# Kernel tuning notes

Measured on AMD Instinct MI355X. Metric: run time of the kernel, lower is better.

Reference implementation:

```python
import jax, jax.numpy as jnp
import numpy as np

N_NODES = 50000
N_EDGES = 800000
IN, HID, OUT = 128, 32, 64
HEADS = (4, 4, 4, 4)  # heads per layer (heads[0], heads[1], heads[1], heads[2])
NEG_SLOPE = 0.2


def gat_layer(h, src, dst, W, al, ar, b, activation):
    """One DGL-style GATConv. h: [N, Din]; W: [Din, H*F]; al, ar: [H, F]; b: [H*F]."""
    n = h.shape[0]
    H, F = al.shape
    feat = (h @ W).reshape(n, H, F)                       # [N, H, F]
    el = jnp.sum(feat * al, axis=-1)                      # [N, H]
    er = jnp.sum(feat * ar, axis=-1)                      # [N, H]
    e = jax.nn.leaky_relu(el[src] + er[dst], NEG_SLOPE)   # [E, H]
    # segment softmax over incoming edges of each dst node
    m = jax.ops.segment_max(e, dst, num_segments=n)       # [N, H]
    ex = jnp.exp(e - m[dst])                              # [E, H]
    denom = jax.ops.segment_sum(ex, dst, num_segments=n)  # [N, H]
    alpha = ex / jnp.maximum(denom[dst], 1e-9)            # [E, H]
    msg = feat[src] * alpha[:, :, None]                   # [E, H, F]
    out = jax.ops.segment_sum(msg, dst, num_segments=n) + b.reshape(H, F)
    return activation(out) if activation is not None else out


def setup_inputs() -> dict:
    key = jax.random.key(0)
    ks = jax.random.split(key, 20)
    x = jax.random.normal(ks[0], (N_NODES, IN), dtype=jnp.float32)
    src = jax.random.randint(ks[1], (N_EDGES,), 0, N_NODES, dtype=jnp.int32)
    dst = jax.random.randint(ks[2], (N_EDGES,), 0, N_NODES, dtype=jnp.int32)
    dims = [(IN, HEADS[0], HID), (HID * HEADS[0], HEADS[1], HID),
            (HID * HEADS[1], HEADS[2], HID), (HID * HEADS[2], HEADS[3], OUT)]
    inp = {"x": x, "src": src, "dst": dst}
    k = 3
    for i, (din, h, f) in enumerate(dims, start=1):
        inp[f"W{i}"] = jax.random.normal(ks[k], (din, h * f), dtype=jnp.float32) * 0.05; k += 1
        inp[f"al{i}"] = jax.random.normal(ks[k], (h, f), dtype=jnp.float32) * 0.05; k += 1
        inp[f"ar{i}"] = jax.random.normal(ks[k], (h, f), dtype=jnp.float32) * 0.05; k += 1
        inp[f"b{i}"] = jnp.zeros((h * f,), dtype=jnp.float32)
    return inp


def reference(x, src, dst, W1, al1, ar1, b1, W2, al2, ar2, b2,
              W3, al3, ar3, b3, W4, al4, ar4, b4):
    elu = jax.nn.elu
    h = gat_layer(x, src, dst, W1, al1, ar1, b1, elu).reshape(N_NODES, -1)   # flatten heads
    h = gat_layer(h, src, dst, W2, al2, ar2, b2, elu).reshape(N_NODES, -1)
    h = gat_layer(h, src, dst, W3, al3, ar3, b3, elu).reshape(N_NODES, -1)
    h = gat_layer(h, src, dst, W4, al4, ar4, b4, None).mean(axis=1)          # mean over heads
    return h
```

## Files before the change

### kernel.cpp

```cpp
#include <hip/hip_runtime.h>
#include <hip/hip_fp16.h>

#define N_NODES 50000
#define N_EDGES 800000

typedef _Float16 h8 __attribute__((ext_vector_type(8)));
typedef float f4 __attribute__((ext_vector_type(4)));

__device__ __forceinline__ float lrelu(float x){ return x > 0.f ? x : 0.2f*x; }
__device__ __forceinline__ float eluf (float x){ return x > 0.f ? x : __expf(x)-1.f; }

__global__ void k_hist(const int* __restrict__ dst, int* __restrict__ cnt){
  int e = blockIdx.x*256 + threadIdx.x;
  if (e < N_EDGES) atomicAdd(&cnt[dst[e]], 1);
}

__global__ void k_scan1(const int* __restrict__ cnt, int* __restrict__ offs, int* __restrict__ bsum){
  __shared__ int tmp[256];
  int tid = threadIdx.x; int i = blockIdx.x*256 + tid;
  int v = (i < N_NODES) ? cnt[i] : 0;
  tmp[tid] = v; __syncthreads();
  for (int d = 1; d < 256; d <<= 1){
    int t = (tid >= d) ? tmp[tid-d] : 0;
    __syncthreads();
    tmp[tid] += t;
    __syncthreads();
  }
  if (i < N_NODES) offs[i] = tmp[tid] - v;
  if (tid == 255) bsum[blockIdx.x] = tmp[tid];
}

__global__ void k_scan2(int* __restrict__ bsum, int nb){
  __shared__ int tmp[256];
  int tid = threadIdx.x;
  int v = (tid < nb) ? bsum[tid] : 0;
  tmp[tid] = v; __syncthreads();
  for (int d = 1; d < 256; d <<= 1){
    int t = (tid >= d) ? tmp[tid-d] : 0;
    __syncthreads();
    tmp[tid] += t;
    __syncthreads();
  }
  if (tid < nb) bsum[tid] = tmp[tid] - v;
}

__global__ void k_scan3(int* __restrict__ offs, const int* __restrict__ bsum, int* __restrict__ cur){
  int i = blockIdx.x*256 + threadIdx.x;
  if (i < N_NODES){
    int o = offs[i] + bsum[blockIdx.x];
    offs[i] = o; cur[i] = o;
  }
  if (i == 0) offs[N_NODES] = N_EDGES;
}

__global__ void k_scatter(const int* __restrict__ src, const int* __restrict__ dst,
                          int* __restrict__ cur, int* __restrict__ csr_src){
  int e = blockIdx.x*256 + threadIdx.x;
  if (e < N_EDGES){
    int pos = atomicAdd(&cur[dst[e]], 1);
    csr_src[pos] = src[e];
  }
}

__global__ void k_wt(const float* __restrict__ W1, const float* __restrict__ W2,
                     const float* __restrict__ W3, const float* __restrict__ W4,
                     _Float16* __restrict__ wt){
  int id = blockIdx.x*256 + threadIdx.x;
  if (id >= 81920) return;
  const float* W; int HF; int loc;
  if (id < 16384)      { W = W1; HF = 128; loc = id; }
  else if (id < 32768) { W = W2; HF = 128; loc = id - 16384; }
  else if (id < 49152) { W = W3; HF = 128; loc = id - 32768; }
  else                 { W = W4; HF = 256; loc = id - 49152; }
  int n = loc >> 7, k = loc & 127;
  wt[id] = (_Float16)W[(size_t)k*HF + n];
}

template<int HF, bool AHALF>
__global__ __launch_bounds__(256) void k_gemm(const void* __restrict__ Ain,
        const _Float16* __restrict__ Wt,
        __half* __restrict__ feat,
        const float* __restrict__ al, const float* __restrict__ ar,
        float* __restrict__ el, float* __restrict__ er){
  __shared__ char lds[49152];
  char* Alds = lds;
  char* Blds = lds + 32768;
  _Float16* Clds = (_Float16*)lds;
  const int tid  = threadIdx.x;
  const int row0 = blockIdx.x * 128;
  const int col0 = blockIdx.y * 64;

  if (AHALF){
    const __half* A16 = (const __half*)Ain;
    #pragma unroll
    for (int i = 0; i < 8; ++i){
      int flat = i*256 + tid;
      int r = flat >> 4, ch = flat & 15;
      uint4 v = make_uint4(0,0,0,0);
      if (row0 + r < N_NODES) v = *(const uint4*)&A16[(size_t)(row0+r)*128 + ch*8];
      *(uint4*)(Alds + ((r*256 + ch*16) ^ ((r&7)<<4))) = v;
    }
  } else {
    const float* A32 = (const float*)Ain;
    #pragma unroll
    for (int i = 0; i < 8; ++i){
      int flat = i*256 + tid;
      int r = flat >> 4, ch = flat & 15;
      h8 hv = {};
      if (row0 + r < N_NODES){
        float4 f0 = *(const float4*)&A32[(size_t)(row0+r)*128 + ch*8];
        float4 f1 = *(const float4*)&A32[(size_t)(row0+r)*128 + ch*8 + 4];
        hv[0]=(_Float16)f0.x; hv[1]=(_Float16)f0.y; hv[2]=(_Float16)f0.z; hv[3]=(_Float16)f0.w;
        hv[4]=(_Float16)f1.x; hv[5]=(_Float16)f1.y; hv[6]=(_Float16)f1.z; hv[7]=(_Float16)f1.w;
      }
      *(h8*)(Alds + ((r*256 + ch*16) ^ ((r&7)<<4))) = hv;
    }
  }
  #pragma unroll
  for (int i = 0; i < 4; ++i){
    int flat = i*256 + tid;
    int n = flat >> 4, ch = flat & 15;
    uint4 v = *(const uint4*)&Wt[(size_t)(col0+n)*128 + ch*8];
    *(uint4*)(Blds + ((n*256 + ch*16) ^ ((n&7)<<4))) = v;
  }
  __syncthreads();

  const int l = tid & 63, w = tid >> 6;
  f4 acc[2][4] = {};
  const int rA0  = w*32 + (l & 15);
  const int rA1  = rA0 + 16;
  const int nB   = (l & 15);
  const int ksel = (l >> 4) * 16;
  #pragma unroll
  for (int kb = 0; kb < 4; ++kb){
    int kofs = kb*64 + ksel;
    h8 a0 = *(const h8*)(Alds + ((rA0*256 + kofs) ^ ((rA0&7)<<4)));
    h8 a1 = *(const h8*)(Alds + ((rA1*256 + kofs) ^ ((rA1&7)<<4)));
    h8 b[4];
    #pragma unroll
    for (int nf = 0; nf < 4; ++nf){
      int n = nB + nf*16;
      b[nf] = *(const h8*)(Blds + ((n*256 + kofs) ^ ((n&7)<<4)));
    }
    #pragma unroll
    for (int nf = 0; nf < 4; ++nf){
      acc[0][nf] = __builtin_amdgcn_mfma_f32_16x16x32_f16(a0, b[nf], acc[0][nf], 0, 0, 0);
      acc[1][nf] = __builtin_amdgcn_mfma_f32_16x16x32_f16(a1, b[nf], acc[1][nf], 0, 0, 0);
    }
  }
  __syncthreads();

  #pragma unroll
  for (int mf = 0; mf < 2; ++mf){
    int rloc = w*32 + mf*16 + (l>>4)*4;
    #pragma unroll
    for (int nf = 0; nf < 4; ++nf){
      int c = nf*16 + (l&15);
      #pragma unroll
      for (int reg = 0; reg < 4; ++reg)
        Clds[(rloc+reg)*80 + c] = (_Float16)acc[mf][nf][reg];
    }
  }
  __syncthreads();

  constexpr int F = HF/4;
  int ch = l & 7;
  float4 al0 = *(const float4*)&al[col0 + ch*8];
  float4 al1 = *(const float4*)&al[col0 + ch*8 + 4];
  float4 ar0 = *(const float4*)&ar[col0 + ch*8];
  float4 ar1 = *(const float4*)&ar[col0 + ch*8 + 4];
  #pragma unroll
  for (int i = 0; i < 4; ++i){
    int rloc = i*32 + w*8 + (l>>3);
    int grow = row0 + rloc;
    h8 hv = *(const h8*)&Clds[rloc*80 + ch*8];
    if (grow < N_NODES)
      *(uint4*)&feat[(size_t)grow*HF + col0 + ch*8] = *(uint4*)&hv;
    float f0=(float)hv[0], f1=(float)hv[1], f2=(float)hv[2], f3=(float)hv[3];
    float f4_=(float)hv[4], f5=(float)hv[5], f6=(float)hv[6], f7=(float)hv[7];
    float pl = f0*al0.x + f1*al0.y + f2*al0.z + f3*al0.w
             + f4_*al1.x + f5*al1.y + f6*al1.z + f7*al1.w;
    float pr = f0*ar0.x + f1*ar0.y + f2*ar0.z + f3*ar0.w
             + f4_*ar1.x + f5*ar1.y + f6*ar1.z + f7*ar1.w;
    pl += __shfl_xor(pl, 1); pl += __shfl_xor(pl, 2);
    pr += __shfl_xor(pr, 1); pr += __shfl_xor(pr, 2);
    if (F == 64){ pl += __shfl_xor(pl, 4); pr += __shfl_xor(pr, 4); }
    bool lead = (F == 32) ? ((l & 3) == 0) : ((l & 7) == 0);
    if (lead && grow < N_NODES){
      int h = (col0 + ch*8) / F;
      el[grow*4 + h] = pl;
      er[grow*4 + h] = pr;
    }
  }
}

template<int F, bool FINAL, int LAYER>
__global__ __launch_bounds__(256) void k_agg(const int* __restrict__ offs,
        const int* __restrict__ csr_src, const float* __restrict__ el,
        const float* __restrict__ er, const __half* __restrict__ feat,
        const float* __restrict__ bias, void* __restrict__ out){
  __shared__ float s_ev[4][64][4];
  __shared__ int   s_src[4][64];
  int tid  = threadIdx.x;
  int wv   = tid >> 6;
  int lane = tid & 63;
  int n = blockIdx.x*4 + wv;
  int beg = offs[n], end = offs[n+1];
  float4 er4 = ((const float4*)er)[n];

  if (F == 32){
    int quarter = lane >> 4;
    int l4      = lane & 15;
    int h       = l4 >> 2;
    float a0=0.f,a1=0.f,a2=0.f,a3=0.f,a4=0.f,a5=0.f,a6=0.f,a7=0.f,ds=0.f;
    for (int cbeg = beg; cbeg < end; cbeg += 64){
      int m = end - cbeg; if (m > 64) m = 64;
      if (lane < m){
        int s = csr_src[cbeg + lane];
        s_src[wv][lane] = s;
        float4 e4 = *(const float4*)&el[(size_t)s*4];
        float4 ev4;
        ev4.x = __expf(lrelu(e4.x + er4.x));
        ev4.y = __expf(lrelu(e4.y + er4.y));
        ev4.z = __expf(lrelu(e4.z + er4.z));
        ev4.w = __expf(lrelu(e4.w + er4.w));
        *(float4*)&s_ev[wv][lane][0] = ev4;
      }
      asm volatile("s_waitcnt lgkmcnt(0)" ::: "memory");
      #pragma unroll 2
      for (int i = 0; i < m; i += 4){
        int e = i + quarter;
        if (e < m){
          int s = s_src[wv][e];
          float ev = s_ev[wv][e][h];
          ds += ev;
          uint4 raw = *(const uint4*)&feat[(size_t)s*128 + l4*8];
          const __half2* hp = reinterpret_cast<const __half2*>(&raw);
          float2 f0 = __half22float2(hp[0]);
          float2 f1 = __half22float2(hp[1]);
          float2 f2 = __half22float2(hp[2]);
          float2 f3 = __half22float2(hp[3]);
          a0 += ev*f0.x; a1 += ev*f0.y; a2 += ev*f1.x; a3 += ev*f1.y;
          a4 += ev*f2.x; a5 += ev*f2.y; a6 += ev*f3.x; a7 += ev*f3.y;
        }
      }
      asm volatile("" ::: "memory");
    }
    ds += __shfl_xor(ds, 16); ds += __shfl_xor(ds, 32);
    a0 += __shfl_xor(a0, 16); a0 += __shfl_xor(a0, 32);
    a1 += __shfl_xor(a1, 16); a1 += __shfl_xor(a1, 32);
    a2 += __shfl_xor(a2, 16); a2 += __shfl_xor(a2, 32);
    a3 += __shfl_xor(a3, 16); a3 += __shfl_xor(a3, 32);
    a4 += __shfl_xor(a4, 16); a4 += __shfl_xor(a4, 32);
    a5 += __shfl_xor(a5, 16); a5 += __shfl_xor(a5, 32);
    a6 += __shfl_xor(a6, 16); a6 += __shfl_xor(a6, 32);
    a7 += __shfl_xor(a7, 16); a7 += __shfl_xor(a7, 32);
    if (quarter == 0){
      float rden = 1.f / fmaxf(ds, 1e-9f);
      float4 b0 = *(const float4*)&bias[l4*8];
      float4 b1 = *(const float4*)&bias[l4*8 + 4];
      float o0 = eluf(a0*rden + b0.x);
      float o1 = eluf(a1*rden + b0.y);
      float o2 = eluf(a2*rden + b0.z);
      float o3 = eluf(a3*rden + b0.w);
      float o4 = eluf(a4*rden + b1.x);
      float o5 = eluf(a5*rden + b1.y);
      float o6 = eluf(a6*rden + b1.z);
      float o7 = eluf(a7*rden + b1.w);
      __half* outh = (__half*)out;
      h8 hv;
      hv[0]=(_Float16)o0; hv[1]=(_Float16)o1; hv[2]=(_Float16)o2; hv[3]=(_Float16)o3;
      hv[4]=(_Float16)o4; hv[5]=(_Float16)o5; hv[6]=(_Float16)o6; hv[7]=(_Float16)o7;
      *(uint4*)&outh[(size_t)n*128 + l4*8] = *(uint4*)&hv;
    }
  } else {
    int hw  = lane >> 5;
    int l5  = lane & 31;
    int h   = l5 >> 3;
    float a0=0.f,a1=0.f,a2=0.f,a3=0.f,a4=0.f,a5=0.f,a6=0.f,a7=0.f,ds=0.f;
    for (int cbeg = beg; cbeg < end; cbeg += 64){
      int m = end - cbeg; if (m > 64) m = 64;
      if (lane < m){
        int s = csr_src[cbeg + lane];
        s_src[wv][lane] = s;
        float4 e4 = *(const float4*)&el[(size_t)s*4];
        float4 ev4;
        ev4.x = __expf(lrelu(e4.x + er4.x));
        ev4.y = __expf(lrelu(e4.y + er4.y));
        ev4.z = __expf(lrelu(e4.z + er4.z));
        ev4.w = __expf(lrelu(e4.w + er4.w));
        *(float4*)&s_ev[wv][lane][0] = ev4;
      }
      asm volatile("s_waitcnt lgkmcnt(0)" ::: "memory");
      #pragma unroll 2
      for (int i = 0; i < m; i += 2){
        int e = i + hw;
        if (e < m){
          int s = s_src[wv][e];
          float ev = s_ev[wv][e][h];
          ds += ev;
          uint4 raw = *(const uint4*)&feat[(size_t)s*256 + l5*8];
          const __half2* hp = reinterpret_cast<const __half2*>(&raw);
          float2 f0 = __half22float2(hp[0]);
          float2 f1 = __half22float2(hp[1]);
          float2 f2 = __half22float2(hp[2]);
          float2 f3 = __half22float2(hp[3]);
          a0 += ev*f0.x; a1 += ev*f0.y; a2 += ev*f1.x; a3 += ev*f1.y;
          a4 += ev*f2.x; a5 += ev*f2.y; a6 += ev*f3.x; a7 += ev*f3.y;
        }
      }
      asm volatile("" ::: "memory");
    }
    ds += __shfl_xor(ds, 32);
    a0 += __shfl_xor(a0, 32); a1 += __shfl_xor(a1, 32);
    a2 += __shfl_xor(a2, 32); a3 += __shfl_xor(a3, 32);
    a4 += __shfl_xor(a4, 32); a5 += __shfl_xor(a5, 32);
    a6 += __shfl_xor(a6, 32); a7 += __shfl_xor(a7, 32);
    float rden = 1.f / fmaxf(ds, 1e-9f);
    float4 b0 = *(const float4*)&bias[l5*8];
    float4 b1 = *(const float4*)&bias[l5*8 + 4];
    float v0 = a0*rden + b0.x;
    float v1 = a1*rden + b0.y;
    float v2 = a2*rden + b0.z;
    float v3 = a3*rden + b0.w;
    float v4 = a4*rden + b1.x;
    float v5 = a5*rden + b1.y;
    float v6 = a6*rden + b1.z;
    float v7 = a7*rden + b1.w;
    v0 += __shfl_xor(v0, 8); v0 += __shfl_xor(v0, 16);
    v1 += __shfl_xor(v1, 8); v1 += __shfl_xor(v1, 16);
    v2 += __shfl_xor(v2, 8); v2 += __shfl_xor(v2, 16);
    v3 += __shfl_xor(v3, 8); v3 += __shfl_xor(v3, 16);
    v4 += __shfl_xor(v4, 8); v4 += __shfl_xor(v4, 16);
    v5 += __shfl_xor(v5, 8); v5 += __shfl_xor(v5, 16);
    v6 += __shfl_xor(v6, 8); v6 += __shfl_xor(v6, 16);
    v7 += __shfl_xor(v7, 8); v7 += __shfl_xor(v7, 16);
    if (hw == 0 && l5 < 8){
      float* outf = (float*)out;
      *(float4*)&outf[(size_t)n*64 + l5*8] =
        make_float4(v0*0.25f, v1*0.25f, v2*0.25f, v3*0.25f);
      *(float4*)&outf[(size_t)n*64 + l5*8 + 4] =
        make_float4(v4*0.25f, v5*0.25f, v6*0.25f, v7*0.25f);
    }
  }
}

extern "C" void kernel_launch(void* const* d_in, const int* in_sizes, int n_in,
                              void* d_out, int out_size, void* d_ws, size_t ws_size,
                              hipStream_t stream){
  const float* x   = (const float*)d_in[0];
  const int*   src = (const int*)  d_in[1];
  const int*   dst = (const int*)  d_in[2];
  const float* W[4]  = {(const float*)d_in[3],  (const float*)d_in[7],
                        (const float*)d_in[11], (const float*)d_in[15]};
  const float* al[4] = {(const float*)d_in[4],  (const float*)d_in[8],
                        (const float*)d_in[12], (const float*)d_in[16]};
  const float* ar[4] = {(const float*)d_in[5],  (const float*)d_in[9],
                        (const float*)d_in[13], (const float*)d_in[17]};
  const float* b[4]  = {(const float*)d_in[6],  (const float*)d_in[10],
                        (const float*)d_in[14], (const float*)d_in[18]};

  char* ws = (char*)d_ws;
  __half*    bufH = (__half*)   (ws);
  __half*    feat = (__half*)   (ws + 25600000);
  _Float16*  wt   = (_Float16*) (ws + 51200000);
  float*     el   = (float*)    (ws + 76800000);
  float*     er   = (float*)    (ws + 77600000);
  int*       offs = (int*)      (ws + 78400000);
  int*       cur  = (int*)      (ws + 78600032);
  int*       bsum = (int*)      (ws + 78800032);
  int*   csr_src  = (int*)      (ws + 78801056);

  (void)hipMemsetAsync(cur, 0, N_NODES*sizeof(int), stream);
  k_hist   <<<3125, 256, 0, stream>>>(dst, cur);
  k_wt     <<<320,  256, 0, stream>>>(W[0], W[1], W[2], W[3], wt);
  k_scan1  <<<196,  256, 0, stream>>>(cur, offs, bsum);
  k_scan2  <<<1,    256, 0, stream>>>(bsum, 196);
  k_scan3  <<<196,  256, 0, stream>>>(offs, bsum, cur);
  k_scatter<<<3125, 256, 0, stream>>>(src, dst, cur, csr_src);

  k_gemm<128,false><<<dim3(391,2), 256, 0, stream>>>(x, wt, feat, al[0], ar[0], el, er);
  k_agg<32,false,1><<<12500, 256, 0, stream>>>(offs, csr_src, el, er, feat, b[0], bufH);

  k_gemm<128,true><<<dim3(391,2), 256, 0, stream>>>(bufH, wt + 16384, feat, al[1], ar[1], el, er);
  k_agg<32,false,2><<<12500, 256, 0, stream>>>(offs, csr_src, el, er, feat, b[1], bufH);

  k_gemm<128,true><<<dim3(391,2), 256, 0, stream>>>(bufH, wt + 32768, feat, al[2], ar[2], el, er);
  k_agg<32,false,3><<<12500, 256, 0, stream>>>(offs, csr_src, el, er, feat, b[2], bufH);

  k_gemm<256,true><<<dim3(391,4), 256, 0, stream>>>(bufH, wt + 49152, feat, al[3], ar[3], el, er);
  k_agg<64,true,4><<<12500, 256, 0, stream>>>(offs, csr_src, el, er, feat, b[3], d_out);
}
```

Baseline: 433.3 us.

## Replace LDS edge staging with register shuffles and fuse hist with weight transpose

The aggregation kernels no longer stage source ids and attention exponentials in shared memory. Each wave now processes 32-edge chunks, with lanes computing one (edge, head) exponential each, and broadcasts values via __shfl. This removes the LDS writes, the waitcnt barrier and the shared-memory footprint, at the cost of more shuffle instructions and a fixed 32-iteration inner loop even for low-degree nodes. Separately, the histogram and weight-transpose kernels are merged into one launch to save a kernel launch.

```diff
diff --git a/kernel.cpp b/kernel.cpp
--- a/kernel.cpp
+++ b/kernel.cpp
@@ -10,9 +10,26 @@
 __device__ __forceinline__ float lrelu(float x){ return x > 0.f ? x : 0.2f*x; }
 __device__ __forceinline__ float eluf (float x){ return x > 0.f ? x : __expf(x)-1.f; }
 
-__global__ void k_hist(const int* __restrict__ dst, int* __restrict__ cnt){
-  int e = blockIdx.x*256 + threadIdx.x;
-  if (e < N_EDGES) atomicAdd(&cnt[dst[e]], 1);
+__global__ void k_histwt(const int* __restrict__ dst, int* __restrict__ cnt,
+                         const float* __restrict__ W1, const float* __restrict__ W2,
+                         const float* __restrict__ W3, const float* __restrict__ W4,
+                         _Float16* __restrict__ wt){
+  int b = blockIdx.x;
+  if (b < 3125){
+    int e = b*256 + threadIdx.x;
+    if (e < N_EDGES) atomicAdd(&cnt[dst[e]], 1);
+  } else {
+    int id = (b - 3125)*256 + threadIdx.x;
+    if (id < 81920){
+      const float* W; int HF; int loc;
+      if (id < 16384)      { W = W1; HF = 128; loc = id; }
+      else if (id < 32768) { W = W2; HF = 128; loc = id - 16384; }
+      else if (id < 49152) { W = W3; HF = 128; loc = id - 32768; }
+      else                 { W = W4; HF = 256; loc = id - 49152; }
+      int n = loc >> 7, k = loc & 127;
+      wt[id] = (_Float16)W[(size_t)k*HF + n];
+    }
+  }
 }
 
 __global__ void k_scan1(const int* __restrict__ cnt, int* __restrict__ offs, int* __restrict__ bsum){
@@ -60,20 +77,6 @@
     int pos = atomicAdd(&cur[dst[e]], 1);
     csr_src[pos] = src[e];
   }
-}
-
-__global__ void k_wt(const float* __restrict__ W1, const float* __restrict__ W2,
-                     const float* __restrict__ W3, const float* __restrict__ W4,
-                     _Float16* __restrict__ wt){
-  int id = blockIdx.x*256 + threadIdx.x;
-  if (id >= 81920) return;
-  const float* W; int HF; int loc;
-  if (id < 16384)      { W = W1; HF = 128; loc = id; }
-  else if (id < 32768) { W = W2; HF = 128; loc = id - 16384; }
-  else if (id < 49152) { W = W3; HF = 128; loc = id - 32768; }
-  else                 { W = W4; HF = 256; loc = id - 49152; }
-  int n = loc >> 7, k = loc & 127;
-  wt[id] = (_Float16)W[(size_t)k*HF + n];
 }
 
 template<int HF, bool AHALF>
@@ -199,40 +202,32 @@
         const int* __restrict__ csr_src, const float* __restrict__ el,
         const float* __restrict__ er, const __half* __restrict__ feat,
         const float* __restrict__ bias, void* __restrict__ out){
-  __shared__ float s_ev[4][64][4];
-  __shared__ int   s_src[4][64];
   int tid  = threadIdx.x;
   int wv   = tid >> 6;
   int lane = tid & 63;
   int n = blockIdx.x*4 + wv;
   int beg = offs[n], end = offs[n+1];
   float4 er4 = ((const float4*)er)[n];
+  int ej = lane & 15, hj = lane >> 4;
+  float er_hj = (hj==0) ? er4.x : (hj==1) ? er4.y : (hj==2) ? er4.z : er4.w;
 
   if (F == 32){
     int quarter = lane >> 4;
     int l4      = lane & 15;
     int h       = l4 >> 2;
     float a0=0.f,a1=0.f,a2=0.f,a3=0.f,a4=0.f,a5=0.f,a6=0.f,a7=0.f,ds=0.f;
-    for (int cbeg = beg; cbeg < end; cbeg += 64){
-      int m = end - cbeg; if (m > 64) m = 64;
-      if (lane < m){
-        int s = csr_src[cbeg + lane];
-        s_src[wv][lane] = s;
-        float4 e4 = *(const float4*)&el[(size_t)s*4];
-        float4 ev4;
-        ev4.x = __expf(lrelu(e4.x + er4.x));
-        ev4.y = __expf(lrelu(e4.y + er4.y));
-        ev4.z = __expf(lrelu(e4.z + er4.z));
-        ev4.w = __expf(lrelu(e4.w + er4.w));
-        *(float4*)&s_ev[wv][lane][0] = ev4;
-      }
-      asm volatile("s_waitcnt lgkmcnt(0)" ::: "memory");
-      #pragma unroll 2
-      for (int i = 0; i < m; i += 4){
+    for (int cbeg = beg; cbeg < end; cbeg += 32){
+      int m = end - cbeg; if (m > 32) m = 32;
+      int sa = 0, sb = 0; float eva = 0.f, evb = 0.f;
+      if (ej < m)      { sa = csr_src[cbeg + ej];      eva = __expf(lrelu(el[sa*4 + hj] + er_hj)); }
+      if (16 + ej < m) { sb = csr_src[cbeg + 16 + ej]; evb = __expf(lrelu(el[sb*4 + hj] + er_hj)); }
+      #pragma unroll 4
+      for (int i = 0; i < 32; i += 4){
         int e = i + quarter;
+        int s; float ev;
+        if (i < 16){ s = __shfl(sa, e & 15); ev = __shfl(eva, (h<<4)|(e & 15)); }
+        else       { s = __shfl(sb, e & 15); ev = __shfl(evb, (h<<4)|(e & 15)); }
         if (e < m){
-          int s = s_src[wv][e];
-          float ev = s_ev[wv][e][h];
           ds += ev;
           uint4 raw = *(const uint4*)&feat[(size_t)s*128 + l4*8];
           const __half2* hp = reinterpret_cast<const __half2*>(&raw);
@@ -244,7 +239,6 @@
           a4 += ev*f2.x; a5 += ev*f2.y; a6 += ev*f3.x; a7 += ev*f3.y;
         }
       }
-      asm volatile("" ::: "memory");
     }
     ds += __shfl_xor(ds, 16); ds += __shfl_xor(ds, 32);
     a0 += __shfl_xor(a0, 16); a0 += __shfl_xor(a0, 32);
@@ -278,26 +272,18 @@
     int l5  = lane & 31;
     int h   = l5 >> 3;
     float a0=0.f,a1=0.f,a2=0.f,a3=0.f,a4=0.f,a5=0.f,a6=0.f,a7=0.f,ds=0.f;
-    for (int cbeg = beg; cbeg < end; cbeg += 64){
-      int m = end - cbeg; if (m > 64) m = 64;
-      if (lane < m){
-        int s = csr_src[cbeg + lane];
-        s_src[wv][lane] = s;
-        float4 e4 = *(const float4*)&el[(size_t)s*4];
-        float4 ev4;
-        ev4.x = __expf(lrelu(e4.x + er4.x));
-        ev4.y = __expf(lrelu(e4.y + er4.y));
-        ev4.z = __expf(lrelu(e4.z + er4.z));
-        ev4.w = __expf(lrelu(e4.w + er4.w));
-        *(float4*)&s_ev[wv][lane][0] = ev4;
-      }
-      asm volatile("s_waitcnt lgkmcnt(0)" ::: "memory");
-      #pragma unroll 2
-      for (int i = 0; i < m; i += 2){
+    for (int cbeg = beg; cbeg < end; cbeg += 32){
+      int m = end - cbeg; if (m > 32) m = 32;
+      int sa = 0, sb = 0; float eva = 0.f, evb = 0.f;
+      if (ej < m)      { sa = csr_src[cbeg + ej];      eva = __expf(lrelu(el[sa*4 + hj] + er_hj)); }
+      if (16 + ej < m) { sb = csr_src[cbeg + 16 + ej]; evb = __expf(lrelu(el[sb*4 + hj] + er_hj)); }
+      #pragma unroll 4
+      for (int i = 0; i < 32; i += 2){
         int e = i + hw;
+        int s; float ev;
+        if (i < 16){ s = __shfl(sa, e & 15); ev = __shfl(eva, (h<<4)|(e & 15)); }
+        else       { s = __shfl(sb, e & 15); ev = __shfl(evb, (h<<4)|(e & 15)); }
         if (e < m){
-          int s = s_src[wv][e];
-          float ev = s_ev[wv][e][h];
           ds += ev;
           uint4 raw = *(const uint4*)&feat[(size_t)s*256 + l5*8];
           const __half2* hp = reinterpret_cast<const __half2*>(&raw);
@@ -309,7 +295,6 @@
           a4 += ev*f2.x; a5 += ev*f2.y; a6 += ev*f3.x; a7 += ev*f3.y;
         }
       }
-      asm volatile("" ::: "memory");
     }
     ds += __shfl_xor(ds, 32);
     a0 += __shfl_xor(a0, 32); a1 += __shfl_xor(a1, 32);
@@ -372,8 +357,7 @@
   int*   csr_src  = (int*)      (ws + 78801056);
 
   (void)hipMemsetAsync(cur, 0, N_NODES*sizeof(int), stream);
-  k_hist   <<<3125, 256, 0, stream>>>(dst, cur);
-  k_wt     <<<320,  256, 0, stream>>>(W[0], W[1], W[2], W[3], wt);
+  k_histwt <<<3445, 256, 0, stream>>>(dst, cur, W[0], W[1], W[2], W[3], wt);
   k_scan1  <<<196,  256, 0, stream>>>(cur, offs, bsum);
   k_scan2  <<<1,    256, 0, stream>>>(bsum, 196);
   k_scan3  <<<196,  256, 0, stream>>>(offs, bsum, cur);
```

Result: slower. 443.7 us (+2.4%).
